# Kernel tuning notes

Measured on AMD Instinct MI355X. Metric: run time of the kernel, lower is better.

## Reference

```python
import jax, jax.numpy as jnp
import numpy as np

D_MODEL = 1024
N_HEADS = 16


def setup_inputs() -> dict:
    key = jax.random.key(0)
    k1, k2, k3, k4, k5 = jax.random.split(key, 5)
    B, L, D = 2, 2048, D_MODEL
    scale = 1.0 / np.sqrt(D)
    return {
        "x": jax.random.normal(k1, (B, L, D), dtype=jnp.float32),
        "W_attn": jax.random.normal(k2, (D, 3 * D), dtype=jnp.float32) * scale,
        "b_attn": jax.random.normal(k3, (3 * D,), dtype=jnp.float32) * 0.02,
        "W_proj": jax.random.normal(k4, (D, D), dtype=jnp.float32) * scale,
        "b_proj": jax.random.normal(k5, (D,), dtype=jnp.float32) * 0.02,
    }


def reference(x, W_attn, b_attn, W_proj, b_proj):
    B, L, D = x.shape
    H = N_HEADS
    Dh = D // H
    qkv = x @ W_attn + b_attn  # [B, L, 3D]
    # Original torch code (faithfully reproduced bug): after splitting q,k,v,
    # q and v are overwritten with k, so q = k = v = the key projection.
    k = qkv[:, :, D:2 * D]
    kh = k.reshape(B, L, H, Dh).transpose(0, 2, 1, 3)  # [B, H, L, Dh]
    att = jnp.einsum("bhqd,bhkd->bhqk", kh, kh) / np.sqrt(Dh)
    att = jax.nn.softmax(att, axis=3)
    out = jnp.einsum("bhqk,bhkd->bhqd", att, kh)  # [B, H, L, Dh]
    out = out.transpose(0, 2, 1, 3).reshape(B, L, D)
    return out @ W_proj + b_proj
```

## Files before the change

### kernel.cpp

```cpp
#include <hip/hip_runtime.h>

#define L_SEQ 2048
#define DM    1024
#define NH    16
#define DH    64
#define BLM   4096

typedef __bf16 bf16x8 __attribute__((ext_vector_type(8)));
typedef float  f32x4  __attribute__((ext_vector_type(4)));

#define MFMA(a,b,c) __builtin_amdgcn_mfma_f32_16x16x32_bf16(a,b,c,0,0,0)

__device__ __forceinline__ unsigned short f2b(float x) {
    unsigned int u = __builtin_bit_cast(unsigned int, x);
    u = (u + 0x7fffu + ((u >> 16) & 1u)) >> 16;
    return (unsigned short)u;
}

typedef __attribute__((address_space(1))) unsigned int GU32;
typedef __attribute__((address_space(3))) unsigned int LU32;
__device__ __forceinline__ void async16(const void* g, void* l) {
    __builtin_amdgcn_global_load_lds((GU32*)g, (LU32*)l, 16, 0, 0);
}

__global__ __launch_bounds__(256) void conv_x(const float* __restrict__ in,
                                              unsigned short* __restrict__ out, int n8) {
    int i = blockIdx.x * 256 + threadIdx.x;
    if (i >= n8) return;
    float4 a = ((const float4*)in)[i * 2];
    float4 b = ((const float4*)in)[i * 2 + 1];
    uint4 v;
    v.x = (unsigned)f2b(a.x) | ((unsigned)f2b(a.y) << 16);
    v.y = (unsigned)f2b(a.z) | ((unsigned)f2b(a.w) << 16);
    v.z = (unsigned)f2b(b.x) | ((unsigned)f2b(b.y) << 16);
    v.w = (unsigned)f2b(b.z) | ((unsigned)f2b(b.w) << 16);
    ((uint4*)out)[i] = v;
}

__global__ __launch_bounds__(256) void transpose_w(const float* __restrict__ W, int ld, int coff,
                                                   unsigned short* __restrict__ out) {
    __shared__ float t[32][33];
    int k0 = blockIdx.x * 32, n0 = blockIdx.y * 32;
    int tx = threadIdx.x & 31, ty = threadIdx.x >> 5;
    #pragma unroll
    for (int i = 0; i < 4; i++) {
        int k = k0 + ty + i * 8;
        t[ty + i * 8][tx] = W[(size_t)k * ld + coff + n0 + tx];
    }
    __syncthreads();
    #pragma unroll
    for (int i = 0; i < 4; i++) {
        int n = n0 + ty + i * 8;
        out[(size_t)n * DM + k0 + tx] = f2b(t[tx][ty + i * 8]);
    }
}

__global__ __launch_bounds__(256) void transpose_k(const unsigned short* __restrict__ kb,
                                                   unsigned short* __restrict__ kt) {
    __shared__ unsigned short t[64][66];
    int l0 = blockIdx.x * 64;
    int bh = blockIdx.y;
    int b = bh >> 4, h = bh & 15;
    int c = threadIdx.x & 63, r4 = threadIdx.x >> 6;
    #pragma unroll
    for (int i = 0; i < 16; i++) {
        int l = r4 + i * 4;
        t[l][c] = kb[(size_t)(b * L_SEQ + l0 + l) * DM + h * DH + c];
    }
    __syncthreads();
    #pragma unroll
    for (int i = 0; i < 16; i++) {
        int d = r4 + i * 4;
        kt[(size_t)(bh * DH + d) * L_SEQ + l0 + c] = t[c][d];
    }
}

template <int OUT_BF16>
__global__ __launch_bounds__(512) void gemm_bt(const unsigned short* __restrict__ A,
                                               const unsigned short* __restrict__ BT,
                                               const float* __restrict__ bias,
                                               void* __restrict__ Cv) {
    __shared__ __align__(16) unsigned short lA[3][128 * 32];
    __shared__ __align__(16) unsigned short lB[3][128 * 32];
    const int old = blockIdx.x + (blockIdx.y << 5);
    const int nl = (old & 7) * 32 + (old >> 3);
    const int bm = nl >> 3, bn = nl & 7;
    const int tid = threadIdx.x, wid = tid >> 6, lane = tid & 63;
    const int wr = wid >> 2, wc = wid & 3;
    const int lg = lane >> 4, lc = lane & 15;
    const int srow = lane >> 2, scol = (lane & 3) * 8;

    f32x4 acc[4][2];
    #pragma unroll
    for (int m = 0; m < 4; m++)
        #pragma unroll
        for (int n = 0; n < 2; n++) acc[m][n] = (f32x4){0.f, 0.f, 0.f, 0.f};

    const unsigned short* gA = A + (size_t)bm * 128 * DM;
    const unsigned short* gB = BT + (size_t)bn * 128 * DM;

#define GSTAGE(buf, kk) do { \
    async16(gA + (size_t)(wid * 16 + srow) * DM + (kk) + scol, lA[buf] + wid * 512); \
    async16(gB + (size_t)(wid * 16 + srow) * DM + (kk) + scol, lB[buf] + wid * 512); \
} while (0)

    GSTAGE(0, 0);
    GSTAGE(1, 32);
    int cur = 0, pre = 2;
    const int NT = DM / 32;
    for (int t = 0; t < NT; ++t) {
        if (t + 1 < NT) asm volatile("s_waitcnt vmcnt(2)\n\ts_barrier" ::: "memory");
        else            asm volatile("s_waitcnt vmcnt(0)\n\ts_barrier" ::: "memory");
        if (t + 2 < NT) GSTAGE(pre, (t + 2) * 32);

        bf16x8 af[4], bfv[2];
        #pragma unroll
        for (int m = 0; m < 4; m++)
            af[m] = *(const bf16x8*)(lA[cur] + (wr * 64 + m * 16 + lc) * 32 + lg * 8);
        #pragma unroll
        for (int n = 0; n < 2; n++)
            bfv[n] = *(const bf16x8*)(lB[cur] + (wc * 32 + n * 16 + lc) * 32 + lg * 8);
        #pragma unroll
        for (int m = 0; m < 4; m++)
            #pragma unroll
            for (int n = 0; n < 2; n++)
                acc[m][n] = MFMA(af[m], bfv[n], acc[m][n]);

        cur = (cur == 2) ? 0 : cur + 1;
        pre = (pre == 2) ? 0 : pre + 1;
    }
#undef GSTAGE

    #pragma unroll
    for (int m = 0; m < 4; m++) {
        int grow = bm * 128 + wr * 64 + m * 16 + lg * 4;
        #pragma unroll
        for (int n = 0; n < 2; n++) {
            int gcol = bn * 128 + wc * 32 + n * 16 + lc;
            float bs = bias[gcol];
            #pragma unroll
            for (int r = 0; r < 4; r++) {
                float v = acc[m][n][r] + bs;
                if (OUT_BF16)
                    ((unsigned short*)Cv)[(size_t)(grow + r) * DM + gcol] = f2b(v);
                else
                    ((float*)Cv)[(size_t)(grow + r) * DM + gcol] = v;
            }
        }
    }
}

__global__ __launch_bounds__(512) void attn_kernel(const unsigned short* __restrict__ kb,
                                                   const unsigned short* __restrict__ kt,
                                                   unsigned short* __restrict__ ob) {
    const int lin = blockIdx.x + (blockIdx.y << 4) + (blockIdx.z << 8);
    const int nl = (lin & 7) * 64 + (lin >> 3);
    const int qblk = nl & 15, h = (nl >> 4) & 15, b = nl >> 8;
    const int tid = threadIdx.x, wid = tid >> 6, lane = tid & 63;
    const int lg = lane >> 4, lc = lane & 15;
    const int q0 = qblk * 128 + wid * 16;
    const int bh = b * NH + h;

    __shared__ __align__(16) unsigned short kT[3][64 * 64];
    __shared__ __align__(16) unsigned short vT[3][64 * 64];
    __shared__ __align__(16) __bf16 p_lds[8][16][72];

    const int srow = wid * 8 + (lane >> 3);
    const int sc = (lane & 7) ^ (srow & 7);
    const unsigned short* gK = kb + (size_t)(b * L_SEQ + srow) * DM + h * DH + sc * 8;
    const unsigned short* gV = kt + (size_t)(bh * DH + srow) * L_SEQ + sc * 8;

    bf16x8 a_q[2];
    {
        const unsigned short* base = kb + (size_t)(b * L_SEQ + q0 + lc) * DM + h * DH;
        a_q[0] = *(const bf16x8*)(base + lg * 8);
        a_q[1] = *(const bf16x8*)(base + 32 + lg * 8);
    }

    bf16x8 ones;
    #pragma unroll
    for (int i = 0; i < 8; i++) ones[i] = (__bf16)1.0f;

    float l_run[4];
    f32x4 o_acc[4];
    #pragma unroll
    for (int r = 0; r < 4; r++) l_run[r] = 0.f;
    #pragma unroll
    for (int dt = 0; dt < 4; dt++) o_acc[dt] = (f32x4){0.f, 0.f, 0.f, 0.f};

    const int NT = L_SEQ / 64;
    async16(gK, &kT[0][wid * 512]);
    async16(gV, &vT[0][wid * 512]);
    async16(gK + (size_t)64 * DM, &kT[1][wid * 512]);
    async16(gV + 64,              &vT[1][wid * 512]);

    int cur = 0, pre = 2;
    for (int t = 0; t < NT; ++t) {
        if (t + 1 < NT) asm volatile("s_waitcnt vmcnt(2)\n\ts_barrier" ::: "memory");
        else            asm volatile("s_waitcnt vmcnt(0)\n\ts_barrier" ::: "memory");
        if (t + 2 < NT) {
            int k0n = (t + 2) * 64;
            async16(gK + (size_t)k0n * DM, &kT[pre][wid * 512]);
            async16(gV + k0n,              &vT[pre][wid * 512]);
        }

        f32x4 s[4];
        #pragma unroll
        for (int nt = 0; nt < 4; nt++) {
            const int r = nt * 16 + lc, x = r & 7;
            const unsigned short* kbase = &kT[cur][r * 64];
            bf16x8 b0 = *(const bf16x8*)(kbase + ((lg    ) ^ x) * 8);
            bf16x8 b1 = *(const bf16x8*)(kbase + ((lg + 4) ^ x) * 8);
            f32x4 a = (f32x4){0.f, 0.f, 0.f, 0.f};
            a = MFMA(a_q[0], b0, a);
            s[nt] = MFMA(a_q[1], b1, a);
        }

        #pragma unroll
        for (int nt = 0; nt < 4; nt++)
            #pragma unroll
            for (int r = 0; r < 4; r++) {
                float p = __expf(__builtin_fmaf(s[nt][r], 0.125f, -16.0f));
                p_lds[wid][lg * 4 + r][nt * 16 + lc] = (__bf16)p;
            }
        asm volatile("s_waitcnt lgkmcnt(0)" ::: "memory");

        f32x4 rs = (f32x4){0.f, 0.f, 0.f, 0.f};
        #pragma unroll
        for (int ks = 0; ks < 2; ks++) {
            bf16x8 ap = *(const bf16x8*)(&p_lds[wid][lc][ks * 32 + lg * 8]);
            rs = MFMA(ap, ones, rs);
            #pragma unroll
            for (int dt = 0; dt < 4; dt++) {
                const int r = dt * 16 + lc, x = r & 7;
                bf16x8 bv = *(const bf16x8*)(&vT[cur][r * 64 + ((ks * 4 + lg) ^ x) * 8]);
                o_acc[dt] = MFMA(ap, bv, o_acc[dt]);
            }
        }
        #pragma unroll
        for (int r = 0; r < 4; r++) l_run[r] += rs[r];

        cur = (cur == 2) ? 0 : cur + 1;
        pre = (pre == 2) ? 0 : pre + 1;
    }

    #pragma unroll
    for (int r = 0; r < 4; r++) {
        float inv = 1.0f / l_run[r];
        int row = q0 + lg * 4 + r;
        unsigned short* orow = ob + (size_t)(b * L_SEQ + row) * DM + h * DH;
        #pragma unroll
        for (int dt = 0; dt < 4; dt++)
            orow[dt * 16 + lc] = f2b(o_acc[dt][r] * inv);
    }
}

extern "C" void kernel_launch(void* const* d_in, const int* in_sizes, int n_in,
                              void* d_out, int out_size, void* d_ws, size_t ws_size,
                              hipStream_t stream) {
    (void)in_sizes; (void)n_in; (void)out_size;
    const float* x      = (const float*)d_in[0];
    const float* W_attn = (const float*)d_in[1];
    const float* b_attn = (const float*)d_in[2];
    const float* W_proj = (const float*)d_in[3];
    const float* b_proj = (const float*)d_in[4];
    float* out = (float*)d_out;

    char* ws = (char*)d_ws;
    const size_t SZ_XB = (size_t)BLM * DM * 2;
    const size_t SZ_W  = (size_t)DM * DM * 2;
    unsigned short* xb  = (unsigned short*)(ws);
    unsigned short* wkT = (unsigned short*)(ws + SZ_XB);
    unsigned short* wpT = (unsigned short*)(ws + SZ_XB + SZ_W);
    unsigned short* kbf = (unsigned short*)(ws + SZ_XB + 2 * SZ_W);
    unsigned short* ktr = (unsigned short*)(ws + 2 * SZ_XB + 2 * SZ_W);
    unsigned short* obf = (unsigned short*)(ws + 3 * SZ_XB + 2 * SZ_W);
    if (ws_size < 4 * SZ_XB + 2 * SZ_W) return;

    conv_x<<<dim3(BLM * DM / 8 / 256), dim3(256), 0, stream>>>(x, xb, BLM * DM / 8);
    transpose_w<<<dim3(32, 32), dim3(256), 0, stream>>>(W_attn, 3 * DM, DM, wkT);
    transpose_w<<<dim3(32, 32), dim3(256), 0, stream>>>(W_proj, DM, 0, wpT);
    gemm_bt<1><<<dim3(32, 8), dim3(512), 0, stream>>>(xb, wkT, b_attn + DM, (void*)kbf);
    transpose_k<<<dim3(L_SEQ / 64, 32), dim3(256), 0, stream>>>(kbf, ktr);
    attn_kernel<<<dim3(L_SEQ / 128, NH, 2), dim3(512), 0, stream>>>(kbf, ktr, obf);
    gemm_bt<0><<<dim3(32, 8), dim3(512), 0, stream>>>(obf, wpT, b_proj, out);
}
```

Before: 183.9 us.

## Keep P in registers via transposed QK^T and retile GEMMs to 64x64

The attention kernel now computes S transposed (K as the A operand), so each lane holds P values in the layout a 16x16x16 MFMA accepts directly. This removes the LDS round trip for P and its waitcnt, and the K-transpose kernel permutes columns to match. The projection GEMMs move from 128x128 tiles with 512 threads to 64x64 tiles with 256 threads, a K-step of 64 and an XOR-swizzled LDS layout. This raises the block count to 1024 for better CU fill, at the cost of less data reuse per tile and twice as many half-width MFMAs in the PV product.

```diff
diff --git a/kernel.cpp b/kernel.cpp
--- a/kernel.cpp
+++ b/kernel.cpp
@@ -7,9 +7,23 @@
 #define BLM   4096
 
 typedef __bf16 bf16x8 __attribute__((ext_vector_type(8)));
+typedef __bf16 bf16x4 __attribute__((ext_vector_type(4)));
+typedef short  s16x4  __attribute__((ext_vector_type(4)));
 typedef float  f32x4  __attribute__((ext_vector_type(4)));
 
 #define MFMA(a,b,c) __builtin_amdgcn_mfma_f32_16x16x32_bf16(a,b,c,0,0,0)
+
+__device__ __forceinline__ f32x4 mfma16(bf16x4 a, bf16x4 b, f32x4 c) {
+#if __has_builtin(__builtin_amdgcn_mfma_f32_16x16x16_bf16)
+    return __builtin_amdgcn_mfma_f32_16x16x16_bf16(a, b, c, 0, 0, 0);
+#elif __has_builtin(__builtin_amdgcn_mfma_f32_16x16x16bf16_1k)
+    return __builtin_amdgcn_mfma_f32_16x16x16bf16_1k(
+        __builtin_bit_cast(s16x4, a), __builtin_bit_cast(s16x4, b), c, 0, 0, 0);
+#else
+    asm("v_mfma_f32_16x16x16_bf16 %0, %1, %2, %3" : "=&v"(c) : "v"(a), "v"(b), "0"(c));
+    return c;
+#endif
+}
 
 __device__ __forceinline__ unsigned short f2b(float x) {
     unsigned int u = __builtin_bit_cast(unsigned int, x);
@@ -68,63 +82,73 @@
         t[l][c] = kb[(size_t)(b * L_SEQ + l0 + l) * DM + h * DH + c];
     }
     __syncthreads();
+    const int cp = ((c >> 2) & 3) * 16 + ((c >> 4) << 2) + (c & 3);
     #pragma unroll
     for (int i = 0; i < 16; i++) {
         int d = r4 + i * 4;
-        kt[(size_t)(bh * DH + d) * L_SEQ + l0 + c] = t[c][d];
+        kt[(size_t)(bh * DH + d) * L_SEQ + l0 + cp] = t[c][d];
     }
 }
 
 template <int OUT_BF16>
-__global__ __launch_bounds__(512) void gemm_bt(const unsigned short* __restrict__ A,
+__global__ __launch_bounds__(256) void gemm_bt(const unsigned short* __restrict__ A,
                                                const unsigned short* __restrict__ BT,
                                                const float* __restrict__ bias,
                                                void* __restrict__ Cv) {
-    __shared__ __align__(16) unsigned short lA[3][128 * 32];
-    __shared__ __align__(16) unsigned short lB[3][128 * 32];
-    const int old = blockIdx.x + (blockIdx.y << 5);
-    const int nl = (old & 7) * 32 + (old >> 3);
-    const int bm = nl >> 3, bn = nl & 7;
+    __shared__ __align__(16) unsigned short lA[3][64 * 64];
+    __shared__ __align__(16) unsigned short lB[3][64 * 64];
+    const int old = blockIdx.x + (blockIdx.y << 6);
+    const int nl = (old & 7) * 128 + (old >> 3);
+    const int bm = nl >> 4, bn = nl & 15;
     const int tid = threadIdx.x, wid = tid >> 6, lane = tid & 63;
-    const int wr = wid >> 2, wc = wid & 3;
+    const int wr = wid >> 1, wc = wid & 1;
     const int lg = lane >> 4, lc = lane & 15;
-    const int srow = lane >> 2, scol = (lane & 3) * 8;
-
-    f32x4 acc[4][2];
-    #pragma unroll
-    for (int m = 0; m < 4; m++)
+    const int sc = (lane & 7) ^ (lane >> 3);
+
+    f32x4 acc[2][2];
+    #pragma unroll
+    for (int m = 0; m < 2; m++)
         #pragma unroll
         for (int n = 0; n < 2; n++) acc[m][n] = (f32x4){0.f, 0.f, 0.f, 0.f};
 
-    const unsigned short* gA = A + (size_t)bm * 128 * DM;
-    const unsigned short* gB = BT + (size_t)bn * 128 * DM;
+    const unsigned short* gA = A + (size_t)bm * 64 * DM;
+    const unsigned short* gB = BT + (size_t)bn * 64 * DM;
 
 #define GSTAGE(buf, kk) do { \
-    async16(gA + (size_t)(wid * 16 + srow) * DM + (kk) + scol, lA[buf] + wid * 512); \
-    async16(gB + (size_t)(wid * 16 + srow) * DM + (kk) + scol, lB[buf] + wid * 512); \
+    async16(gA + (size_t)(wid * 8 + (lane >> 3)) * DM + (kk) + sc * 8,      lA[buf] + (wid * 8) * 64 + lane * 8); \
+    async16(gA + (size_t)(32 + wid * 8 + (lane >> 3)) * DM + (kk) + sc * 8, lA[buf] + (32 + wid * 8) * 64 + lane * 8); \
+    async16(gB + (size_t)(wid * 8 + (lane >> 3)) * DM + (kk) + sc * 8,      lB[buf] + (wid * 8) * 64 + lane * 8); \
+    async16(gB + (size_t)(32 + wid * 8 + (lane >> 3)) * DM + (kk) + sc * 8, lB[buf] + (32 + wid * 8) * 64 + lane * 8); \
 } while (0)
 
     GSTAGE(0, 0);
-    GSTAGE(1, 32);
+    GSTAGE(1, 64);
     int cur = 0, pre = 2;
-    const int NT = DM / 32;
+    const int NT = DM / 64;
     for (int t = 0; t < NT; ++t) {
-        if (t + 1 < NT) asm volatile("s_waitcnt vmcnt(2)\n\ts_barrier" ::: "memory");
+        if (t + 1 < NT) asm volatile("s_waitcnt vmcnt(4)\n\ts_barrier" ::: "memory");
         else            asm volatile("s_waitcnt vmcnt(0)\n\ts_barrier" ::: "memory");
-        if (t + 2 < NT) GSTAGE(pre, (t + 2) * 32);
-
-        bf16x8 af[4], bfv[2];
-        #pragma unroll
-        for (int m = 0; m < 4; m++)
-            af[m] = *(const bf16x8*)(lA[cur] + (wr * 64 + m * 16 + lc) * 32 + lg * 8);
-        #pragma unroll
-        for (int n = 0; n < 2; n++)
-            bfv[n] = *(const bf16x8*)(lB[cur] + (wc * 32 + n * 16 + lc) * 32 + lg * 8);
-        #pragma unroll
-        for (int m = 0; m < 4; m++)
-            #pragma unroll
-            for (int n = 0; n < 2; n++)
-                acc[m][n] = MFMA(af[m], bfv[n], acc[m][n]);
+        if (t + 2 < NT) GSTAGE(pre, (t + 2) * 64);
+
+        #pragma unroll
+        for (int ks = 0; ks < 2; ks++) {
+            bf16x8 af[2], bfv[2];
+            #pragma unroll
+            for (int m = 0; m < 2; m++) {
+                int row = wr * 32 + m * 16 + lc;
+                af[m] = *(const bf16x8*)(lA[cur] + row * 64 + ((ks * 4 + lg) ^ (lc & 7)) * 8);
+            }
+            #pragma unroll
+            for (int n = 0; n < 2; n++) {
+                int row = wc * 32 + n * 16 + lc;
+                bfv[n] = *(const bf16x8*)(lB[cur] + row * 64 + ((ks * 4 + lg) ^ (lc & 7)) * 8);
+            }
+            #pragma unroll
+            for (int m = 0; m < 2; m++)
+                #pragma unroll
+                for (int n = 0; n < 2; n++)
+                    acc[m][n] = MFMA(af[m], bfv[n], acc[m][n]);
+        }
 
         cur = (cur == 2) ? 0 : cur + 1;
         pre = (pre == 2) ? 0 : pre + 1;
@@ -132,11 +156,11 @@
 #undef GSTAGE
 
     #pragma unroll
-    for (int m = 0; m < 4; m++) {
-        int grow = bm * 128 + wr * 64 + m * 16 + lg * 4;
+    for (int m = 0; m < 2; m++) {
+        int grow = bm * 64 + wr * 32 + m * 16 + lg * 4;
         #pragma unroll
         for (int n = 0; n < 2; n++) {
-            int gcol = bn * 128 + wc * 32 + n * 16 + lc;
+            int gcol = bn * 64 + wc * 32 + n * 16 + lc;
             float bs = bias[gcol];
             #pragma unroll
             for (int r = 0; r < 4; r++) {
@@ -163,7 +187,6 @@
 
     __shared__ __align__(16) unsigned short kT[3][64 * 64];
     __shared__ __align__(16) unsigned short vT[3][64 * 64];
-    __shared__ __align__(16) __bf16 p_lds[8][16][72];
 
     const int srow = wid * 8 + (lane >> 3);
     const int sc = (lane & 7) ^ (srow & 7);
@@ -177,14 +200,12 @@
         a_q[1] = *(const bf16x8*)(base + 32 + lg * 8);
     }
 
-    bf16x8 ones;
-    #pragma unroll
-    for (int i = 0; i < 8; i++) ones[i] = (__bf16)1.0f;
-
-    float l_run[4];
+    bf16x4 ones4;
+    #pragma unroll
+    for (int i = 0; i < 4; i++) ones4[i] = (__bf16)1.0f;
+
+    f32x4 l_acc = (f32x4){0.f, 0.f, 0.f, 0.f};
     f32x4 o_acc[4];
-    #pragma unroll
-    for (int r = 0; r < 4; r++) l_run[r] = 0.f;
     #pragma unroll
     for (int dt = 0; dt < 4; dt++) o_acc[dt] = (f32x4){0.f, 0.f, 0.f, 0.f};
 
@@ -209,36 +230,38 @@
         for (int nt = 0; nt < 4; nt++) {
             const int r = nt * 16 + lc, x = r & 7;
             const unsigned short* kbase = &kT[cur][r * 64];
-            bf16x8 b0 = *(const bf16x8*)(kbase + ((lg    ) ^ x) * 8);
-            bf16x8 b1 = *(const bf16x8*)(kbase + ((lg + 4) ^ x) * 8);
+            bf16x8 k0v = *(const bf16x8*)(kbase + ((lg    ) ^ x) * 8);
+            bf16x8 k1v = *(const bf16x8*)(kbase + ((lg + 4) ^ x) * 8);
             f32x4 a = (f32x4){0.f, 0.f, 0.f, 0.f};
-            a = MFMA(a_q[0], b0, a);
-            s[nt] = MFMA(a_q[1], b1, a);
-        }
-
+            a = MFMA(k0v, a_q[0], a);
+            s[nt] = MFMA(k1v, a_q[1], a);
+        }
+
+        bf16x4 pa[4];
         #pragma unroll
         for (int nt = 0; nt < 4; nt++)
             #pragma unroll
             for (int r = 0; r < 4; r++) {
                 float p = __expf(__builtin_fmaf(s[nt][r], 0.125f, -16.0f));
-                p_lds[wid][lg * 4 + r][nt * 16 + lc] = (__bf16)p;
-            }
-        asm volatile("s_waitcnt lgkmcnt(0)" ::: "memory");
-
-        f32x4 rs = (f32x4){0.f, 0.f, 0.f, 0.f};
-        #pragma unroll
-        for (int ks = 0; ks < 2; ks++) {
-            bf16x8 ap = *(const bf16x8*)(&p_lds[wid][lc][ks * 32 + lg * 8]);
-            rs = MFMA(ap, ones, rs);
-            #pragma unroll
-            for (int dt = 0; dt < 4; dt++) {
-                const int r = dt * 16 + lc, x = r & 7;
-                bf16x8 bv = *(const bf16x8*)(&vT[cur][r * 64 + ((ks * 4 + lg) ^ x) * 8]);
-                o_acc[dt] = MFMA(ap, bv, o_acc[dt]);
-            }
-        }
-        #pragma unroll
-        for (int r = 0; r < 4; r++) l_run[r] += rs[r];
+                pa[nt][r] = (__bf16)p;
+            }
+
+        #pragma unroll
+        for (int nt = 0; nt < 4; nt++) l_acc = mfma16(pa[nt], ones4, l_acc);
+
+        #pragma unroll
+        for (int dt = 0; dt < 4; dt++) {
+            const int row = dt * 16 + lc, x = lc & 7;
+            const unsigned short* vbase = &vT[cur][row * 64];
+            #pragma unroll
+            for (int hh = 0; hh < 2; hh++) {
+                bf16x8 vb = *(const bf16x8*)(vbase + ((lg * 2 + hh) ^ x) * 8);
+                bf16x4 vlo = __builtin_shufflevector(vb, vb, 0, 1, 2, 3);
+                bf16x4 vhi = __builtin_shufflevector(vb, vb, 4, 5, 6, 7);
+                o_acc[dt] = mfma16(pa[hh * 2],     vlo, o_acc[dt]);
+                o_acc[dt] = mfma16(pa[hh * 2 + 1], vhi, o_acc[dt]);
+            }
+        }
 
         cur = (cur == 2) ? 0 : cur + 1;
         pre = (pre == 2) ? 0 : pre + 1;
@@ -246,7 +269,7 @@
 
     #pragma unroll
     for (int r = 0; r < 4; r++) {
-        float inv = 1.0f / l_run[r];
+        float inv = 1.0f / l_acc[r];
         int row = q0 + lg * 4 + r;
         unsigned short* orow = ob + (size_t)(b * L_SEQ + row) * DM + h * DH;
         #pragma unroll
@@ -280,8 +303,8 @@
     conv_x<<<dim3(BLM * DM / 8 / 256), dim3(256), 0, stream>>>(x, xb, BLM * DM / 8);
     transpose_w<<<dim3(32, 32), dim3(256), 0, stream>>>(W_attn, 3 * DM, DM, wkT);
     transpose_w<<<dim3(32, 32), dim3(256), 0, stream>>>(W_proj, DM, 0, wpT);
-    gemm_bt<1><<<dim3(32, 8), dim3(512), 0, stream>>>(xb, wkT, b_attn + DM, (void*)kbf);
+    gemm_bt<1><<<dim3(64, 16), dim3(256), 0, stream>>>(xb, wkT, b_attn + DM, (void*)kbf);
     transpose_k<<<dim3(L_SEQ / 64, 32), dim3(256), 0, stream>>>(kbf, ktr);
     attn_kernel<<<dim3(L_SEQ / 128, NH, 2), dim3(512), 0, stream>>>(kbf, ktr, obf);
-    gemm_bt<0><<<dim3(32, 8), dim3(512), 0, stream>>>(obf, wpT, b_proj, out);
-}
+    gemm_bt<0><<<dim3(64, 16), dim3(256), 0, stream>>>(obf, wpT, b_proj, out);
+}
```

Result: no change. 182.7 us (-0.7%).
